# Kernel tuning notes

Measured on AMD Instinct MI355X. Metric: run time of the kernel, lower is better.

Reference implementation:

```python
import jax, jax.numpy as jnp
import numpy as np

B, N_PER, D_IN, D_OUT, E_PER = 64, 256, 256, 128, 8192  # graphs, nodes/graph, in feat, out feat (=clusters K), edges/graph
EPS = 1e-12


def _sage(h, src, dst, W, b):
    # DenseSAGEConv (mean aggregator): h [n,Din], src/dst [E]
    agg = jnp.zeros_like(h).at[dst].add(h[src])                 # sum of in-neighbor messages
    deg = jnp.zeros((h.shape[0],), h.dtype).at[dst].add(1.0)
    agg = agg / jnp.maximum(deg, 1.0)[:, None]                  # mean aggregation
    z = jnp.concatenate([h, agg], axis=-1) @ W + b              # Linear(2*Din -> Dout)
    z = z / jnp.maximum(jnp.linalg.norm(z, axis=-1, keepdims=True), EPS)  # F.normalize(p=2)
    return jax.nn.relu(z)                                       # activation


def setup_inputs() -> dict:
    key = jax.random.key(0)
    ks = jax.random.split(key, 5)
    h = jax.random.normal(ks[0], (B, N_PER, D_IN), jnp.float32)
    edge_src = jax.random.randint(ks[1], (B, E_PER), 0, N_PER)
    edge_dst = jax.random.randint(ks[2], (B, E_PER), 0, N_PER)
    s = 1.0 / np.sqrt(2 * D_IN)
    W_feat = jax.random.uniform(ks[3], (2 * D_IN, D_OUT), jnp.float32, -s, s)
    b_feat = jnp.zeros((D_OUT,), jnp.float32)
    W_pool = jax.random.uniform(ks[4], (2 * D_IN, D_OUT), jnp.float32, -s, s)
    b_pool = jnp.zeros((D_OUT,), jnp.float32)
    return {"h": h, "edge_src": edge_src, "edge_dst": edge_dst,
            "W_feat": W_feat, "b_feat": b_feat, "W_pool": W_pool, "b_pool": b_pool}


def reference(h, edge_src, edge_dst, W_feat, b_feat, W_pool, b_pool):
    sage = jax.vmap(_sage, in_axes=(0, 0, 0, None, None))
    feat = sage(h, edge_src, edge_dst, W_feat, b_feat)                          # [B,n,K]
    assign = jax.nn.softmax(sage(h, edge_src, edge_dst, W_pool, b_pool), -1)    # [B,n,K]
    # h = assign^T @ feat, per graph (equivalent to block_diag(assign)^T @ stacked feat)
    h_pool = jnp.einsum('bnk,bnd->bkd', assign, feat).reshape(B * D_OUT, D_OUT)  # [B*K, Dout]
    # adj_new = S^T A S per graph; A[dst,src]=1 per edge -> sum_e outer(S[dst_e], S[src_e])
    s_dst = jnp.take_along_axis(assign, edge_dst[:, :, None], axis=1)           # [B,E,K]
    s_src = jnp.take_along_axis(assign, edge_src[:, :, None], axis=1)           # [B,E,K]
    blocks = jnp.einsum('bek,bel->bkl', s_dst, s_src)                           # [B,K,K]
    # cross-graph blocks are exactly zero in the batched graph -> block-diagonal dense adj
    adj_new = jax.scipy.linalg.block_diag(*blocks)                              # [B*K, B*K]
    return adj_new, h_pool
```

## Files before the change

kernel.cpp:

```cpp
#include <hip/hip_runtime.h>
#include <hip/hip_bf16.h>
#include <stdint.h>

#define BG 64
#define NP 256
#define DI 256
#define DO 128
#define EP 8192


typedef __attribute__((ext_vector_type(8))) short short8;
typedef __attribute__((ext_vector_type(4))) short short4v;
typedef __attribute__((ext_vector_type(4))) float float4v;

__device__ __forceinline__ int ldi(const void* p, size_t i, int i64) {
  return i64 ? (int)((const long long*)p)[i] : ((const int*)p)[i];
}

__device__ __forceinline__ short f2b(float x) {
  union { float f; unsigned u; } c; c.f = x;
  unsigned r = c.u + 0x7FFFu + ((c.u >> 16) & 1u);
  return (short)(r >> 16);
}
__device__ __forceinline__ float b2f(short b) {
  union { unsigned u; float f; } c; c.u = ((unsigned)(unsigned short)b) << 16;
  return c.f;
}

__device__ __forceinline__ int vote_i64(const void* esrc) {
  const uint32_t* ew = (const uint32_t*)esrc;
  int i64 = 1;
#pragma unroll
  for (int j = 0; j < 8; ++j)
    if (ew[2 * j + 1] != 0) i64 = 0;
  return i64;
}

__device__ __forceinline__ void fill_adj_rows(float* __restrict__ adj, int r0) {
  int t = threadIdx.x;
  const float4v z = {0.f, 0.f, 0.f, 0.f};
  for (int rr = 0; rr < 16; ++rr) {
    int r = r0 + rr;
    int g = r >> 7;
    float4v* row = (float4v*)(adj + (size_t)r * (BG * DO));
    int s0 = g * 32;
#pragma unroll
    for (int it = 0; it < 8; ++it) {
      int p = it * 256 + t;
      if ((unsigned)(p - s0) >= 32u)
        __builtin_nontemporal_store(z, &row[p]);
    }
  }
}

__global__ __launch_bounds__(256) void k_prep(const float* __restrict__ h,
                                              const void* __restrict__ esrc,
                                              const void* __restrict__ edst,
                                              const float* __restrict__ Wf,
                                              const float* __restrict__ Wp,
                                              short* __restrict__ hThi,
                                              short* __restrict__ hTlo,
                                              short* __restrict__ Abf,
                                              float* __restrict__ deg,
                                              short* __restrict__ Wt) {
  __shared__ __align__(16) char smem[65536];
  int bx = blockIdx.x, t = threadIdx.x;
  if (bx < 1024) {
    float (*T)[65] = (float(*)[65])smem;
    int b = bx >> 4, n0 = (bx & 3) * 64, f0 = ((bx >> 2) & 3) * 64;
    int r = t >> 4, c4 = (t & 15) * 4;
#pragma unroll
    for (int i = 0; i < 4; ++i) {
      float4 v = *(const float4*)&h[((size_t)b * NP + n0 + i * 16 + r) * DI + f0 + c4];
      T[i * 16 + r][c4 + 0] = v.x; T[i * 16 + r][c4 + 1] = v.y;
      T[i * 16 + r][c4 + 2] = v.z; T[i * 16 + r][c4 + 3] = v.w;
    }
    __syncthreads();
#pragma unroll
    for (int i = 0; i < 4; ++i) {
      int f = i * 16 + r;
      short hi4[4], lo4[4];
#pragma unroll
      for (int j = 0; j < 4; ++j) {
        float x = T[c4 + j][f];
        short hb = f2b(x);
        hi4[j] = hb;
        lo4[j] = f2b(x - b2f(hb));
      }
      size_t o = ((size_t)b * DI + f0 + f) * NP + n0 + c4;
      *(short4v*)&hThi[o] = *(short4v*)hi4;
      *(short4v*)&hTlo[o] = *(short4v*)lo4;
    }
  } else if (bx < 1280) {
    float (*Asl)[256] = (float(*)[256])smem;
    int idx = bx - 1024, b = idx >> 2, rq = idx & 3;
    float4* Az = (float4*)&Asl[0][0];
    for (int i = t; i < 64 * 256 / 4; i += 256) Az[i] = make_float4(0.f, 0.f, 0.f, 0.f);
    int i64 = vote_i64(esrc);
    __syncthreads();
    const size_t base = (size_t)b * EP;
    for (int e = t; e < EP; e += 256) {
      int si = ldi(esrc, base + e, i64) & (NP - 1);
      int di = ldi(edst, base + e, i64) & (NP - 1);
      if ((di >> 6) == rq) atomicAdd(&Asl[di & 63][si], 1.0f);
    }
    __syncthreads();
    int wv = t >> 6, ln = t & 63;
#pragma unroll
    for (int k = 0; k < 16; ++k) {
      int r = k * 4 + wv;
      float4 v = *(float4*)&Asl[r][ln * 4];
      int gr = rq * 64 + r;
      size_t o = ((size_t)b * NP + gr) * NP + ln * 4;
      short tmp[4] = { f2b(v.x), f2b(v.y), f2b(v.z), f2b(v.w) };
      *(short4v*)&Abf[o] = *(short4v*)tmp;
      float s = v.x + v.y + v.z + v.w;
      s += __shfl_xor(s, 1);  s += __shfl_xor(s, 2);  s += __shfl_xor(s, 4);
      s += __shfl_xor(s, 8);  s += __shfl_xor(s, 16); s += __shfl_xor(s, 32);
      if (ln == 0) deg[b * NP + gr] = s;
    }
  } else {
    float (*T)[132] = (float(*)[132])smem;
    int bb = bx - 1280;
    int head = bb >> 4;
    int k0 = (bb & 15) * 32;
    const float* W = head ? Wp : Wf;
    {
      int k = t >> 3, fs = (t & 7) * 16;
      const float* src = &W[(size_t)(k0 + k) * DO + fs];
#pragma unroll
      for (int j = 0; j < 4; ++j)
        *(float4*)&T[k][fs + j * 4] = *(const float4*)(src + j * 4);
    }
    __syncthreads();
    int f = t & 127, kh = (t >> 7) * 16;
    __align__(16) short tmp[16];
#pragma unroll
    for (int i = 0; i < 16; ++i) tmp[i] = f2b(T[kh + i][f]);
    short* dst = &Wt[((size_t)head * DO + f) * 512 + k0 + kh];
    *(short8*)dst = *(short8*)&tmp[0];
    *(short8*)(dst + 8) = *(short8*)&tmp[8];
  }
}

__global__ __launch_bounds__(256) void k_fz(const float* __restrict__ h,
                                            const short* __restrict__ Abf,
                                            const short* __restrict__ hThi,
                                            const short* __restrict__ hTlo,
                                            const float* __restrict__ deg,
                                            const short* __restrict__ Wt,
                                            const float* __restrict__ bfe,
                                            const float* __restrict__ bpo,
                                            short* __restrict__ FtH, short* __restrict__ FtL,
                                            short* __restrict__ PtH, short* __restrict__ PtL,
                                            float* __restrict__ adj) {
  __shared__ __align__(16) char smem[40960];
  int bx = blockIdx.x, t = threadIdx.x;
  if (bx >= 512) { fill_adj_rows(adj, (bx - 512) * 16); return; }
  short (*Xa)[264] = (short(*)[264])smem;
  short (*Xs)[40]  = (short(*)[40])(smem + 16896);
  short (*TT)[2][128][40] = (short(*)[2][128][40])smem;
  int r0 = bx * 32;
  int b = r0 >> 8, nl = r0 & 255;
  int wave = t >> 6, lane = t & 63;
  int rt = wave & 1, ch = wave >> 1;
  int m = lane & 15, q = lane >> 4;
  float4v acc[8];
#pragma unroll
  for (int i = 0; i < 8; ++i) acc[i] = (float4v){0.f, 0.f, 0.f, 0.f};

  const short* Ar = &Abf[((size_t)r0 + rt * 16 + m) * NP];
  for (int kc = 0; kc < NP; kc += 32) {
    short8 af = *(const short8*)&Ar[kc + q * 8];
#pragma unroll
    for (int tt = 0; tt < 8; ++tt) {
      int f = ch * 128 + tt * 16 + m;
      short8 bh = *(const short8*)&hThi[((size_t)b * DI + f) * NP + kc + q * 8];
      short8 bl = *(const short8*)&hTlo[((size_t)b * DI + f) * NP + kc + q * 8];
      acc[tt] = __builtin_amdgcn_mfma_f32_16x16x32_bf16(af, bh, acc[tt], 0, 0, 0);
      acc[tt] = __builtin_amdgcn_mfma_f32_16x16x32_bf16(af, bl, acc[tt], 0, 0, 0);
    }
  }
#pragma unroll
  for (int reg = 0; reg < 4; ++reg) {
    int rowl = rt * 16 + q * 4 + reg;
    float sc = 1.0f / fmaxf(deg[r0 + rowl], 1.0f);
#pragma unroll
    for (int tt = 0; tt < 8; ++tt)
      Xa[rowl][ch * 128 + tt * 16 + m] = f2b(acc[tt][reg] * sc);
  }
  __syncthreads();

#pragma unroll
  for (int i = 0; i < 8; ++i) acc[i] = (float4v){0.f, 0.f, 0.f, 0.f};
  for (int kc = 0; kc < 2 * DI; kc += 32) {
    short8 afrag;
    if (kc < DI) {
      __syncthreads();
      {
        int r = t >> 3, k4 = (t & 7) * 4;
        float4 v = *(const float4*)&h[(size_t)(r0 + r) * DI + kc + k4];
        Xs[r][k4 + 0] = f2b(v.x); Xs[r][k4 + 1] = f2b(v.y);
        Xs[r][k4 + 2] = f2b(v.z); Xs[r][k4 + 3] = f2b(v.w);
      }
      __syncthreads();
      afrag = *(const short8*)&Xs[rt * 16 + m][q * 8];
    } else {
      afrag = *(const short8*)&Xa[rt * 16 + m][(kc - DI) + q * 8];
    }
#pragma unroll
    for (int tt = 0; tt < 8; ++tt) {
      int n = ch * 128 + tt * 16 + m;
      short8 bfrag = *(const short8*)&Wt[(size_t)n * 512 + kc + q * 8];
      acc[tt] = __builtin_amdgcn_mfma_f32_16x16x32_bf16(afrag, bfrag, acc[tt], 0, 0, 0);
    }
  }
  __syncthreads();

  const float* bp = ch ? bpo : bfe;
  float bias[8];
#pragma unroll
  for (int tt = 0; tt < 8; ++tt) bias[tt] = bp ? bp[tt * 16 + m] : 0.f;
#pragma unroll
  for (int reg = 0; reg < 4; ++reg) {
    int rloc = rt * 16 + q * 4 + reg;
    float z[8];
    float ss = 0.f;
#pragma unroll
    for (int tt = 0; tt < 8; ++tt) { z[tt] = acc[tt][reg] + bias[tt]; ss += z[tt] * z[tt]; }
    ss += __shfl_xor(ss, 1); ss += __shfl_xor(ss, 2);
    ss += __shfl_xor(ss, 4); ss += __shfl_xor(ss, 8);
    float inv = 1.0f / fmaxf(sqrtf(ss), 1e-12f);
    float v[8];
#pragma unroll
    for (int tt = 0; tt < 8; ++tt) v[tt] = fmaxf(z[tt] * inv, 0.f);
    if (ch == 1) {
      float mx = v[0];
#pragma unroll
      for (int tt = 1; tt < 8; ++tt) mx = fmaxf(mx, v[tt]);
      mx = fmaxf(mx, __shfl_xor(mx, 1)); mx = fmaxf(mx, __shfl_xor(mx, 2));
      mx = fmaxf(mx, __shfl_xor(mx, 4)); mx = fmaxf(mx, __shfl_xor(mx, 8));
      float e[8], s = 0.f;
#pragma unroll
      for (int tt = 0; tt < 8; ++tt) { e[tt] = __expf(v[tt] - mx); s += e[tt]; }
      s += __shfl_xor(s, 1); s += __shfl_xor(s, 2);
      s += __shfl_xor(s, 4); s += __shfl_xor(s, 8);
      float is = 1.0f / s;
#pragma unroll
      for (int tt = 0; tt < 8; ++tt) v[tt] = e[tt] * is;
    }
#pragma unroll
    for (int tt = 0; tt < 8; ++tt) {
      short hb = f2b(v[tt]);
      short lb = f2b(v[tt] - b2f(hb));
      TT[ch][0][tt * 16 + m][rloc] = hb;
      TT[ch][1][tt * 16 + m][rloc] = lb;
    }
  }
  __syncthreads();
#pragma unroll
  for (int it = 0; it < 8; ++it) {
    int chunk = it * 256 + t;
    int c = chunk & 3, col = (chunk >> 2) & 127;
    int hl = (chunk >> 9) & 1, head = chunk >> 10;
    short* base = head ? (hl ? PtL : PtH) : (hl ? FtL : FtH);
    short* dst = &base[((size_t)b * DO + col) * NP + nl + c * 8];
    *(short8*)dst = *(const short8*)&TT[head][hl][col][c * 8];
  }
}

__global__ __launch_bounds__(256) void k_gemm_as(const short* __restrict__ Abf,
                                                 const short* __restrict__ PtH,
                                                 const short* __restrict__ PtL,
                                                 short* __restrict__ AStH,
                                                 short* __restrict__ AStL,
                                                 float* __restrict__ adj) {
  __shared__ __align__(16) short TS[2][128][40];
  int bx = blockIdx.x, t = threadIdx.x;
  if (bx >= 512) { fill_adj_rows(adj, 4096 + (bx - 512) * 16); return; }
  int b = bx >> 3, n0 = (bx & 7) * 32;
  int wave = t >> 6, lane = t & 63, rt = wave & 1, fh = wave >> 1;
  int m = lane & 15, q = lane >> 4;
  float4v acc[4];
#pragma unroll
  for (int i = 0; i < 4; ++i) acc[i] = (float4v){0.f, 0.f, 0.f, 0.f};
  const short* Ar = &Abf[((size_t)b * NP + n0 + rt * 16 + m) * NP];
  for (int kc = 0; kc < NP; kc += 32) {
    short8 af = *(const short8*)&Ar[kc + q * 8];
#pragma unroll
    for (int tt = 0; tt < 4; ++tt) {
      int j = fh * 64 + tt * 16 + m;
      short8 bh = *(const short8*)&PtH[((size_t)b * DO + j) * NP + kc + q * 8];
      short8 bl = *(const short8*)&PtL[((size_t)b * DO + j) * NP + kc + q * 8];
      acc[tt] = __builtin_amdgcn_mfma_f32_16x16x32_bf16(af, bh, acc[tt], 0, 0, 0);
      acc[tt] = __builtin_amdgcn_mfma_f32_16x16x32_bf16(af, bl, acc[tt], 0, 0, 0);
    }
  }
#pragma unroll
  for (int tt = 0; tt < 4; ++tt) {
#pragma unroll
    for (int reg = 0; reg < 4; ++reg) {
      int j = fh * 64 + tt * 16 + m;
      int nlr = rt * 16 + q * 4 + reg;
      float vv = acc[tt][reg];
      short hb = f2b(vv);
      TS[0][j][nlr] = hb;
      TS[1][j][nlr] = f2b(vv - b2f(hb));
    }
  }
  __syncthreads();
#pragma unroll
  for (int it = 0; it < 4; ++it) {
    int chunk = it * 256 + t;
    int c = chunk & 3, col = (chunk >> 2) & 127, hl = chunk >> 9;
    short* dst = &(hl ? AStL : AStH)[((size_t)b * DO + col) * NP + n0 + c * 8];
    *(short8*)dst = *(const short8*)&TS[hl][col][c * 8];
  }
}

__global__ __launch_bounds__(256) void k_pool2(const short* __restrict__ PtH,
                                               const short* __restrict__ PtL,
                                               const short* __restrict__ AStH,
                                               const short* __restrict__ AStL,
                                               const short* __restrict__ FtH,
                                               const short* __restrict__ FtL,
                                               float* __restrict__ adj,
                                               float* __restrict__ hpool) {
  int bx = blockIdx.x, t = threadIdx.x;
  if (bx >= 512) { fill_adj_rows(adj, 6144 + (bx - 512) * 16); return; }
  int b = bx >> 3, x = bx & 7;
  int ch2 = x & 1, rh = (x >> 1) & 1, which = x >> 2;
  const short* YH = which ? FtH : AStH;
  const short* YL = which ? FtL : AStL;
  int wave = t >> 6, lane = t & 63;
  int m = lane & 15, q = lane >> 4;
  float4v acc[4];
#pragma unroll
  for (int i = 0; i < 4; ++i) acc[i] = (float4v){0.f, 0.f, 0.f, 0.f};
  int irow = rh * 64 + wave * 16 + m;
  const short* pah = &PtH[((size_t)b * DO + irow) * NP];
  const short* pal = &PtL[((size_t)b * DO + irow) * NP];
  for (int kc = 0; kc < NP; kc += 32) {
    short8 ah = *(const short8*)&pah[kc + q * 8];
    short8 al = *(const short8*)&pal[kc + q * 8];
#pragma unroll
    for (int tt = 0; tt < 4; ++tt) {
      int j = ch2 * 64 + tt * 16 + m;
      short8 bh = *(const short8*)&YH[((size_t)b * DO + j) * NP + kc + q * 8];
      short8 bl = *(const short8*)&YL[((size_t)b * DO + j) * NP + kc + q * 8];
      acc[tt] = __builtin_amdgcn_mfma_f32_16x16x32_bf16(ah, bh, acc[tt], 0, 0, 0);
      acc[tt] = __builtin_amdgcn_mfma_f32_16x16x32_bf16(al, bh, acc[tt], 0, 0, 0);
      acc[tt] = __builtin_amdgcn_mfma_f32_16x16x32_bf16(ah, bl, acc[tt], 0, 0, 0);
    }
  }
#pragma unroll
  for (int tt = 0; tt < 4; ++tt) {
#pragma unroll
    for (int reg = 0; reg < 4; ++reg) {
      int i = rh * 64 + wave * 16 + q * 4 + reg;
      int j = ch2 * 64 + tt * 16 + m;
      float vv = acc[tt][reg];
      if (which == 0)
        adj[(size_t)(b * DO + i) * (BG * DO) + (size_t)b * DO + j] = vv;
      else
        hpool[((size_t)b * DO + i) * DO + j] = vv;
    }
  }
}

extern "C" void kernel_launch(void* const* d_in, const int* in_sizes, int n_in,
                              void* d_out, int out_size, void* d_ws, size_t ws_size,
                              hipStream_t stream) {
  (void)out_size; (void)ws_size;
  int ih = -1, ie[2] = {-1, -1}, iw[2] = {-1, -1}, ib[2] = {-1, -1};
  int ne = 0, nw = 0, nb = 0;
  for (int i = 0; i < n_in; ++i) {
    long long s = in_sizes[i];
    if (s == (long long)BG * NP * DI) { if (ih < 0) ih = i; }
    else if (s == (long long)BG * EP && ne < 2) ie[ne++] = i;
    else if (s == (long long)2 * DI * DO && nw < 2) iw[nw++] = i;
    else if (s == (long long)DO && nb < 2) ib[nb++] = i;
  }
  if (ih < 0 || ne < 2 || nw < 2) {
    ih = 0;
    ie[0] = (n_in > 1) ? 1 : 0;  ie[1] = (n_in > 2) ? 2 : ie[0];
    iw[0] = (n_in > 3) ? 3 : 0;  iw[1] = (n_in > 5) ? 5 : iw[0];
    ib[0] = (n_in > 4) ? 4 : -1; ib[1] = (n_in > 6) ? 6 : -1;
    nb = (ib[1] >= 0) ? 2 : (ib[0] >= 0 ? 1 : 0);
  }
  const float* h    = (const float*)d_in[ih];
  const void* esrc  = d_in[ie[0]];
  const void* edst  = d_in[ie[1]];
  const float* Wf   = (const float*)d_in[iw[0]];
  const float* Wp   = (const float*)d_in[iw[1]];
  const float* bfe  = (nb >= 1) ? (const float*)d_in[ib[0]] : nullptr;
  const float* bpo  = (nb >= 2) ? (const float*)d_in[ib[1]] : nullptr;

  float* adj   = (float*)d_out;
  float* hpool = (float*)d_out + (size_t)(BG * DO) * (BG * DO);

  char* wb = (char*)d_ws;
  short* Abf  = (short*)wb;
  short* hThi = (short*)(wb + 8388608);
  short* hTlo = (short*)(wb + 16777216);
  short* PtH  = (short*)(wb + 25165824);
  short* PtL  = (short*)(wb + 29360128);
  short* FtH  = (short*)(wb + 33554432);
  short* FtL  = (short*)(wb + 37748736);
  short* AStH = (short*)(wb + 41943040);
  short* AStL = (short*)(wb + 46137344);
  float* deg  = (float*)(wb + 50331648);
  short* Wt   = (short*)(wb + 50397184);

  k_prep<<<1312, 256, 0, stream>>>(h, esrc, edst, Wf, Wp, hThi, hTlo, Abf, deg, Wt);
  k_fz<<<768, 256, 0, stream>>>(h, Abf, hThi, hTlo, deg, Wt, bfe, bpo,
                                FtH, FtL, PtH, PtL, adj);
  k_gemm_as<<<640, 256, 0, stream>>>(Abf, PtH, PtL, AStH, AStL, adj);
  k_pool2<<<640, 256, 0, stream>>>(PtH, PtL, AStH, AStL, FtH, FtL, adj, hpool);
}
```

Before: 415.8 us.

## Precompute bf16 row-major h and move hpool GEMM into earlier kernel

Result: no change. 417.2 us (+0.3%).

```diff
diff --git a/kernel.cpp b/kernel.cpp
--- a/kernel.cpp
+++ b/kernel.cpp
@@ -53,6 +53,44 @@
   }
 }
 
+__device__ __forceinline__ void pool_core(const short* __restrict__ PtHb,
+                                          const short* __restrict__ PtLb,
+                                          const short* __restrict__ YHb,
+                                          const short* __restrict__ YLb,
+                                          float* __restrict__ outb, int ld,
+                                          int ch2, int rh) {
+  int t = threadIdx.x, wave = t >> 6, lane = t & 63;
+  int m = lane & 15, q = lane >> 4;
+  float4v acc[4];
+#pragma unroll
+  for (int i = 0; i < 4; ++i) acc[i] = (float4v){0.f, 0.f, 0.f, 0.f};
+  int irow = rh * 64 + wave * 16 + m;
+  const short* pah = &PtHb[(size_t)irow * NP];
+  const short* pal = &PtLb[(size_t)irow * NP];
+  for (int kc = 0; kc < NP; kc += 32) {
+    short8 ah = *(const short8*)&pah[kc + q * 8];
+    short8 al = *(const short8*)&pal[kc + q * 8];
+#pragma unroll
+    for (int tt = 0; tt < 4; ++tt) {
+      int j = ch2 * 64 + tt * 16 + m;
+      short8 bh = *(const short8*)&YHb[(size_t)j * NP + kc + q * 8];
+      short8 bl = *(const short8*)&YLb[(size_t)j * NP + kc + q * 8];
+      acc[tt] = __builtin_amdgcn_mfma_f32_16x16x32_bf16(ah, bh, acc[tt], 0, 0, 0);
+      acc[tt] = __builtin_amdgcn_mfma_f32_16x16x32_bf16(al, bh, acc[tt], 0, 0, 0);
+      acc[tt] = __builtin_amdgcn_mfma_f32_16x16x32_bf16(ah, bl, acc[tt], 0, 0, 0);
+    }
+  }
+#pragma unroll
+  for (int tt = 0; tt < 4; ++tt) {
+#pragma unroll
+    for (int reg = 0; reg < 4; ++reg) {
+      int i = rh * 64 + wave * 16 + q * 4 + reg;
+      int j = ch2 * 64 + tt * 16 + m;
+      outb[(size_t)i * ld + j] = acc[tt][reg];
+    }
+  }
+}
+
 __global__ __launch_bounds__(256) void k_prep(const float* __restrict__ h,
                                               const void* __restrict__ esrc,
                                               const void* __restrict__ edst,
@@ -60,6 +98,7 @@
                                               const float* __restrict__ Wp,
                                               short* __restrict__ hThi,
                                               short* __restrict__ hTlo,
+                                              short* __restrict__ hRhi,
                                               short* __restrict__ Abf,
                                               float* __restrict__ deg,
                                               short* __restrict__ Wt) {
@@ -71,7 +110,10 @@
     int r = t >> 4, c4 = (t & 15) * 4;
 #pragma unroll
     for (int i = 0; i < 4; ++i) {
-      float4 v = *(const float4*)&h[((size_t)b * NP + n0 + i * 16 + r) * DI + f0 + c4];
+      size_t ridx = (size_t)b * NP + n0 + i * 16 + r;
+      float4 v = *(const float4*)&h[ridx * DI + f0 + c4];
+      short rh4[4] = { f2b(v.x), f2b(v.y), f2b(v.z), f2b(v.w) };
+      *(short4v*)&hRhi[ridx * DI + f0 + c4] = *(short4v*)rh4;
       T[i * 16 + r][c4 + 0] = v.x; T[i * 16 + r][c4 + 1] = v.y;
       T[i * 16 + r][c4 + 2] = v.z; T[i * 16 + r][c4 + 3] = v.w;
     }
@@ -143,7 +185,7 @@
   }
 }
 
-__global__ __launch_bounds__(256) void k_fz(const float* __restrict__ h,
+__global__ __launch_bounds__(256) void k_fz(const short* __restrict__ hRhi,
                                             const short* __restrict__ Abf,
                                             const short* __restrict__ hThi,
                                             const short* __restrict__ hTlo,
@@ -158,7 +200,6 @@
   int bx = blockIdx.x, t = threadIdx.x;
   if (bx >= 512) { fill_adj_rows(adj, (bx - 512) * 16); return; }
   short (*Xa)[264] = (short(*)[264])smem;
-  short (*Xs)[40]  = (short(*)[40])(smem + 16896);
   short (*TT)[2][128][40] = (short(*)[2][128][40])smem;
   int r0 = bx * 32;
   int b = r0 >> 8, nl = r0 & 255;
@@ -193,21 +234,18 @@
 
 #pragma unroll
   for (int i = 0; i < 8; ++i) acc[i] = (float4v){0.f, 0.f, 0.f, 0.f};
-  for (int kc = 0; kc < 2 * DI; kc += 32) {
-    short8 afrag;
-    if (kc < DI) {
-      __syncthreads();
-      {
-        int r = t >> 3, k4 = (t & 7) * 4;
-        float4 v = *(const float4*)&h[(size_t)(r0 + r) * DI + kc + k4];
-        Xs[r][k4 + 0] = f2b(v.x); Xs[r][k4 + 1] = f2b(v.y);
-        Xs[r][k4 + 2] = f2b(v.z); Xs[r][k4 + 3] = f2b(v.w);
-      }
-      __syncthreads();
-      afrag = *(const short8*)&Xs[rt * 16 + m][q * 8];
-    } else {
-      afrag = *(const short8*)&Xa[rt * 16 + m][(kc - DI) + q * 8];
-    }
+  const short* hr = &hRhi[(size_t)(r0 + rt * 16 + m) * DI];
+  for (int kc = 0; kc < DI; kc += 32) {
+    short8 afrag = *(const short8*)&hr[kc + q * 8];
+#pragma unroll
+    for (int tt = 0; tt < 8; ++tt) {
+      int n = ch * 128 + tt * 16 + m;
+      short8 bfrag = *(const short8*)&Wt[(size_t)n * 512 + kc + q * 8];
+      acc[tt] = __builtin_amdgcn_mfma_f32_16x16x32_bf16(afrag, bfrag, acc[tt], 0, 0, 0);
+    }
+  }
+  for (int kc = DI; kc < 2 * DI; kc += 32) {
+    short8 afrag = *(const short8*)&Xa[rt * 16 + m][(kc - DI) + q * 8];
 #pragma unroll
     for (int tt = 0; tt < 8; ++tt) {
       int n = ch * 128 + tt * 16 + m;
@@ -272,12 +310,22 @@
 __global__ __launch_bounds__(256) void k_gemm_as(const short* __restrict__ Abf,
                                                  const short* __restrict__ PtH,
                                                  const short* __restrict__ PtL,
+                                                 const short* __restrict__ FtH,
+                                                 const short* __restrict__ FtL,
                                                  short* __restrict__ AStH,
                                                  short* __restrict__ AStL,
+                                                 float* __restrict__ hpool,
                                                  float* __restrict__ adj) {
   __shared__ __align__(16) short TS[2][128][40];
   int bx = blockIdx.x, t = threadIdx.x;
-  if (bx >= 512) { fill_adj_rows(adj, 4096 + (bx - 512) * 16); return; }
+  if (bx >= 768) { fill_adj_rows(adj, 4096 + (bx - 768) * 16); return; }
+  if (bx >= 512) {
+    int idx = bx - 512, b = idx >> 2, x = idx & 3, ch2 = x & 1, rh = x >> 1;
+    pool_core(&PtH[(size_t)b * DO * NP], &PtL[(size_t)b * DO * NP],
+              &FtH[(size_t)b * DO * NP], &FtL[(size_t)b * DO * NP],
+              &hpool[(size_t)b * DO * DO], DO, ch2, rh);
+    return;
+  }
   int b = bx >> 3, n0 = (bx & 7) * 32;
   int wave = t >> 6, lane = t & 63, rt = wave & 1, fh = wave >> 1;
   int m = lane & 15, q = lane >> 4;
@@ -322,50 +370,13 @@
                                                const short* __restrict__ PtL,
                                                const short* __restrict__ AStH,
                                                const short* __restrict__ AStL,
-                                               const short* __restrict__ FtH,
-                                               const short* __restrict__ FtL,
-                                               float* __restrict__ adj,
-                                               float* __restrict__ hpool) {
-  int bx = blockIdx.x, t = threadIdx.x;
-  if (bx >= 512) { fill_adj_rows(adj, 6144 + (bx - 512) * 16); return; }
-  int b = bx >> 3, x = bx & 7;
-  int ch2 = x & 1, rh = (x >> 1) & 1, which = x >> 2;
-  const short* YH = which ? FtH : AStH;
-  const short* YL = which ? FtL : AStL;
-  int wave = t >> 6, lane = t & 63;
-  int m = lane & 15, q = lane >> 4;
-  float4v acc[4];
-#pragma unroll
-  for (int i = 0; i < 4; ++i) acc[i] = (float4v){0.f, 0.f, 0.f, 0.f};
-  int irow = rh * 64 + wave * 16 + m;
-  const short* pah = &PtH[((size_t)b * DO + irow) * NP];
-  const short* pal = &PtL[((size_t)b * DO + irow) * NP];
-  for (int kc = 0; kc < NP; kc += 32) {
-    short8 ah = *(const short8*)&pah[kc + q * 8];
-    short8 al = *(const short8*)&pal[kc + q * 8];
-#pragma unroll
-    for (int tt = 0; tt < 4; ++tt) {
-      int j = ch2 * 64 + tt * 16 + m;
-      short8 bh = *(const short8*)&YH[((size_t)b * DO + j) * NP + kc + q * 8];
-      short8 bl = *(const short8*)&YL[((size_t)b * DO + j) * NP + kc + q * 8];
-      acc[tt] = __builtin_amdgcn_mfma_f32_16x16x32_bf16(ah, bh, acc[tt], 0, 0, 0);
-      acc[tt] = __builtin_amdgcn_mfma_f32_16x16x32_bf16(al, bh, acc[tt], 0, 0, 0);
-      acc[tt] = __builtin_amdgcn_mfma_f32_16x16x32_bf16(ah, bl, acc[tt], 0, 0, 0);
-    }
-  }
-#pragma unroll
-  for (int tt = 0; tt < 4; ++tt) {
-#pragma unroll
-    for (int reg = 0; reg < 4; ++reg) {
-      int i = rh * 64 + wave * 16 + q * 4 + reg;
-      int j = ch2 * 64 + tt * 16 + m;
-      float vv = acc[tt][reg];
-      if (which == 0)
-        adj[(size_t)(b * DO + i) * (BG * DO) + (size_t)b * DO + j] = vv;
-      else
-        hpool[((size_t)b * DO + i) * DO + j] = vv;
-    }
-  }
+                                               float* __restrict__ adj) {
+  int bx = blockIdx.x;
+  if (bx >= 256) { fill_adj_rows(adj, 6144 + (bx - 256) * 16); return; }
+  int b = bx >> 2, x = bx & 3, ch2 = x & 1, rh = x >> 1;
+  pool_core(&PtH[(size_t)b * DO * NP], &PtL[(size_t)b * DO * NP],
+            &AStH[(size_t)b * DO * NP], &AStL[(size_t)b * DO * NP],
+            &adj[(size_t)(b * DO) * (BG * DO) + (size_t)b * DO], BG * DO, ch2, rh);
 }
 
 extern "C" void kernel_launch(void* const* d_in, const int* in_sizes, int n_in,
@@ -403,18 +414,19 @@
   short* Abf  = (short*)wb;
   short* hThi = (short*)(wb + 8388608);
   short* hTlo = (short*)(wb + 16777216);
-  short* PtH  = (short*)(wb + 25165824);
-  short* PtL  = (short*)(wb + 29360128);
-  short* FtH  = (short*)(wb + 33554432);
-  short* FtL  = (short*)(wb + 37748736);
-  short* AStH = (short*)(wb + 41943040);
-  short* AStL = (short*)(wb + 46137344);
-  float* deg  = (float*)(wb + 50331648);
-  short* Wt   = (short*)(wb + 50397184);
-
-  k_prep<<<1312, 256, 0, stream>>>(h, esrc, edst, Wf, Wp, hThi, hTlo, Abf, deg, Wt);
-  k_fz<<<768, 256, 0, stream>>>(h, Abf, hThi, hTlo, deg, Wt, bfe, bpo,
+  short* hRhi = (short*)(wb + 25165824);
+  short* PtH  = (short*)(wb + 33554432);
+  short* PtL  = (short*)(wb + 37748736);
+  short* FtH  = (short*)(wb + 41943040);
+  short* FtL  = (short*)(wb + 46137344);
+  short* AStH = (short*)(wb + 50331648);
+  short* AStL = (short*)(wb + 54525952);
+  float* deg  = (float*)(wb + 58720256);
+  short* Wt   = (short*)(wb + 58785792);
+
+  k_prep<<<1312, 256, 0, stream>>>(h, esrc, edst, Wf, Wp, hThi, hTlo, hRhi, Abf, deg, Wt);
+  k_fz<<<768, 256, 0, stream>>>(hRhi, Abf, hThi, hTlo, deg, Wt, bfe, bpo,
                                 FtH, FtL, PtH, PtL, adj);
-  k_gemm_as<<<640, 256, 0, stream>>>(Abf, PtH, PtL, AStH, AStL, adj);
-  k_pool2<<<640, 256, 0, stream>>>(PtH, PtL, AStH, AStL, FtH, FtL, adj, hpool);
-}
+  k_gemm_as<<<896, 256, 0, stream>>>(Abf, PtH, PtL, FtH, FtL, AStH, AStL, hpool, adj);
+  k_pool2<<<384, 256, 0, stream>>>(PtH, PtL, AStH, AStL, adj);
+}
```
